# Performance work log

Hardware: AMD Instinct MI355X
Metric: run time of the kernel (lower is better)

The kernel has to match this reference:

```python
import jax, jax.numpy as jnp
import numpy as np

HID = 2048      # hidden_size
NH = 32         # num_heads
QLR = 1536      # q_lora_rank
KVLR = 512      # kv_lora_rank
DR = 64         # qk_rope_head_dim
DN = 128        # qk_nope_head_dim
DV = 128        # v_head_dim
DQK = DN + DR   # 192
EPS = 1e-6
ROPE_BASE = 10000.0


def rms_norm(x, w):
    return x * jax.lax.rsqrt(jnp.mean(x * x, axis=-1, keepdims=True) + EPS) * w


def apply_rope(x, pos):
    # x: [B, S, H, d] (non-interleaved / rotate-half convention), pos: [S]
    d = x.shape[-1]
    inv_freq = 1.0 / (ROPE_BASE ** (jnp.arange(0, d, 2, dtype=jnp.float32) / d))
    freqs = pos[:, None].astype(jnp.float32) * inv_freq      # [S, d/2]
    cos = jnp.cos(freqs)[None, :, None, :]                   # [1, S, 1, d/2]
    sin = jnp.sin(freqs)[None, :, None, :]
    x1, x2 = x[..., : d // 2], x[..., d // 2:]
    return jnp.concatenate([x1 * cos - x2 * sin, x1 * sin + x2 * cos], axis=-1)


def setup_inputs() -> dict:
    key = jax.random.key(0)
    ks = jax.random.split(key, 8)
    s = 0.02
    return {
        "hidden_states": jax.random.normal(ks[0], (1, 2048, HID), jnp.float32),
        "q_a_w":    jax.random.normal(ks[1], (HID, QLR), jnp.float32) * s,
        "q_a_ln_w": jnp.ones((QLR,), jnp.float32),
        "q_b_w":    jax.random.normal(ks[2], (QLR, NH * DQK), jnp.float32) * s,
        "kv_a_w":   jax.random.normal(ks[3], (HID, KVLR + DR), jnp.float32) * s,
        "kv_a_ln_w": jnp.ones((KVLR,), jnp.float32),
        "kv_b_w":   jax.random.normal(ks[4], (KVLR, NH * (DN + DV)), jnp.float32) * s,
        "o_w":      jax.random.normal(ks[5], (NH * DV, HID), jnp.float32) * s,
    }


def reference(hidden_states, q_a_w, q_a_ln_w, q_b_w, kv_a_w, kv_a_ln_w, kv_b_w, o_w):
    B, S, _ = hidden_states.shape
    # low-rank Q: down-proj -> RMSNorm -> up-proj
    q = rms_norm(hidden_states @ q_a_w, q_a_ln_w) @ q_b_w       # [B,S,NH*DQK]
    q = q.reshape(B, S, NH, DQK)
    q_pass, q_rot = q[..., :DN], q[..., DN:]
    # compressed KV + shared rope key
    ckv = hidden_states @ kv_a_w                                # [B,S,KVLR+DR]
    c_kv, k_rot = ckv[..., :KVLR], ckv[..., KVLR:]
    kv = rms_norm(c_kv, kv_a_ln_w) @ kv_b_w                     # [B,S,NH*(DN+DV)]
    kv = kv.reshape(B, S, NH, DN + DV)
    k_pass, v = kv[..., :DN], kv[..., DN:]
    # RoPE
    pos = jnp.arange(S)
    q_rot = apply_rope(q_rot, pos)                              # [B,S,NH,DR]
    k_rot = apply_rope(k_rot[:, :, None, :], pos)[:, :, 0, :]   # [B,S,DR] (shared head)
    # causal attention, scale = qk_head_dim**-0.5
    scale = DQK ** -0.5
    scores = (jnp.einsum('bqhd,bkhd->bhqk', q_pass, k_pass)
              + jnp.einsum('bqhd,bkd->bhqk', q_rot, k_rot)) * scale
    causal = jnp.tril(jnp.ones((S, S), dtype=bool))
    scores = jnp.where(causal[None, None], scores, jnp.finfo(scores.dtype).min)
    p = jax.nn.softmax(scores, axis=-1)
    out = jnp.einsum('bhqk,bkhd->bqhd', p, v).reshape(B, S, NH * DV)
    return out @ o_w
```

## Files before the change

kernel.cpp:

```cpp
#include <hip/hip_runtime.h>


typedef __bf16 bf16x8 __attribute__((ext_vector_type(8)));
typedef float  f32x4  __attribute__((ext_vector_type(4)));
typedef unsigned u32x4 __attribute__((ext_vector_type(4)));

#define GLOAD16(g, l)                                                          \
  __builtin_amdgcn_global_load_lds(                                            \
      (const __attribute__((address_space(1))) unsigned int*)(g),              \
      (__attribute__((address_space(3))) unsigned int*)(l), 16, 0, 0)

__device__ __forceinline__ unsigned short f2b(float f) {
  unsigned u = __builtin_bit_cast(unsigned, f);
  u += 0x7fffu + ((u >> 16) & 1u);
  return (unsigned short)(u >> 16);
}

__device__ __forceinline__ float b2f(unsigned short u) {
  return __builtin_bit_cast(float, (unsigned)u << 16);
}

__device__ __forceinline__ unsigned cvtpk(float lo, float hi) {
  unsigned r;
  asm("v_cvt_pk_bf16_f32 %0, %1, %2" : "=v"(r) : "v"(lo), "v"(hi));
  return r;
}

__device__ __forceinline__ void tc_body(const float* __restrict__ src,
                                        unsigned short* __restrict__ dst,
                                        int R, int C, int bx, int by,
                                        int tx, int ty) {
  __shared__ float t[32][33];
  int r0 = bx * 32, c0 = by * 32;
#pragma unroll
  for (int j = 0; j < 4; j++) {
    int c = c0 + tx;
    t[ty + j * 8][tx] = (c < C) ? src[(size_t)(r0 + ty + j * 8) * C + c] : 0.f;
  }
  __syncthreads();
#pragma unroll
  for (int j = 0; j < 4; j++)
    dst[(size_t)(c0 + ty + j * 8) * R + r0 + tx] = f2b(t[tx][ty + j * 8]);
}

__global__ __launch_bounds__(256) void prep(
    const float* __restrict__ hs, unsigned short* __restrict__ hs_b,
    const float* __restrict__ qaw, const float* __restrict__ kvaw,
    unsigned short* __restrict__ wcat,
    const float* __restrict__ qbw, unsigned short* __restrict__ qbT,
    const float* __restrict__ kvbw, unsigned short* __restrict__ kvbT,
    const float* __restrict__ ow, unsigned short* __restrict__ owT) {
  int b = blockIdx.x;
  int tid = threadIdx.x;
  if (b < 4096) {
    int i = b * 256 + tid;
    float4 v = ((const float4*)hs)[i];
    ushort4 o;
    o.x = f2b(v.x); o.y = f2b(v.y); o.z = f2b(v.z); o.w = f2b(v.w);
    ((ushort4*)hs_b)[i] = o;
    return;
  }
  b -= 4096;
  int tx = tid & 31, ty = tid >> 5;
  if (b < 3072)       { tc_body(qaw,  wcat,               2048, 1536, b & 63,  b >> 6, tx, ty); return; }
  b -= 3072;
  if (b < 1280)       { tc_body(kvaw, wcat + 1536UL*2048, 2048, 576,  b & 63,  b >> 6, tx, ty); return; }
  b -= 1280;
  if (b < 9216)       { tc_body(qbw,  qbT,                1536, 6144, b % 48,  b / 48, tx, ty); return; }
  b -= 9216;
  if (b < 4096)       { tc_body(kvbw, kvbT,               512,  8192, b & 15,  b >> 4, tx, ty); return; }
  b -= 4096;
  tc_body(ow, owT, 4096, 2048, b & 127, b >> 7, tx, ty);
}

__global__ __launch_bounds__(256) void rms2(const float* __restrict__ c0,
                                            const float* __restrict__ c1,
                                            const float* __restrict__ qw,
                                            const float* __restrict__ kvw,
                                            unsigned short* __restrict__ qan,
                                            unsigned short* __restrict__ ckvn,
                                            unsigned short* __restrict__ Kb) {
  int b = blockIdx.x, tid = threadIdx.x;
  __shared__ float red[4];
  if (b < 2048) {
    const float* x0 = c0 + (size_t)b * 2176;
    const float* x1 = c1 + (size_t)b * 2176;
    float vb[6], ss = 0.f;
#pragma unroll
    for (int j = 0; j < 6; j++) {
      float v = x0[tid + j * 256] + x1[tid + j * 256];
      vb[j] = v; ss += v * v;
    }
#pragma unroll
    for (int off = 1; off < 64; off <<= 1) ss += __shfl_xor(ss, off, 64);
    if ((tid & 63) == 0) red[tid >> 6] = ss;
    __syncthreads();
    ss = red[0] + red[1] + red[2] + red[3];
    float r = rsqrtf(ss / 1536.f + 1e-6f);
    unsigned short* orow = qan + (size_t)b * 1536;
#pragma unroll
    for (int j = 0; j < 6; j++)
      orow[tid + j * 256] = f2b(vb[j] * r * qw[tid + j * 256]);
  } else {
    int t = b - 2048;
    const float* x0 = c0 + (size_t)t * 2176 + 1536;
    const float* x1 = c1 + (size_t)t * 2176 + 1536;
    float vb[2], ss = 0.f;
#pragma unroll
    for (int j = 0; j < 2; j++) {
      float v = x0[tid + j * 256] + x1[tid + j * 256];
      vb[j] = v; ss += v * v;
    }
#pragma unroll
    for (int off = 1; off < 64; off <<= 1) ss += __shfl_xor(ss, off, 64);
    __shared__ unsigned short rot[64];
    if ((tid & 63) == 0) red[tid >> 6] = ss;
    __syncthreads();
    ss = red[0] + red[1] + red[2] + red[3];
    float r = rsqrtf(ss / 512.f + 1e-6f);
    unsigned short* orow = ckvn + (size_t)t * 512;
#pragma unroll
    for (int j = 0; j < 2; j++)
      orow[tid + j * 256] = f2b(vb[j] * r * kvw[tid + j * 256]);
    if (tid < 32) {
      float x1v = c0[(size_t)t * 2176 + 2048 + tid] + c1[(size_t)t * 2176 + 2048 + tid];
      float x2v = c0[(size_t)t * 2176 + 2080 + tid] + c1[(size_t)t * 2176 + 2080 + tid];
      float a = (float)t * exp2f(-(float)tid * 0.4152410118609203f);
      float cs = __cosf(a), sn = __sinf(a);
      rot[tid]      = f2b(x1v * cs - x2v * sn);
      rot[tid + 32] = f2b(x1v * sn + x2v * cs);
    }
    __syncthreads();
    for (int idx = tid; idx < 2048; idx += 256) {
      int h = idx >> 6, d = idx & 63;
      Kb[(size_t)t * 6144 + h * 192 + 128 + d] = rot[d];
    }
  }
}

__global__ __launch_bounds__(256) void addout(const float4* __restrict__ p,
                                              float4* __restrict__ o) {
  int i = blockIdx.x * 256 + threadIdx.x;
  float4 a = p[i], b = p[i + 1048576], c = p[i + 2097152], d = p[i + 3145728];
  float4 r;
  r.x = (a.x + b.x) + (c.x + d.x);
  r.y = (a.y + b.y) + (c.y + d.y);
  r.z = (a.z + b.z) + (c.z + d.z);
  r.w = (a.w + b.w) + (c.w + d.w);
  o[i] = r;
}

__global__ __launch_bounds__(256) void gemm_bt(const unsigned short* __restrict__ A,
                                               const unsigned short* __restrict__ Bt,
                                               float* __restrict__ Cp,
                                               int M, int N, int Ktot,
                                               int GX, int total, int splits) {
  __shared__ unsigned short As[4096];
  __shared__ unsigned short Bs[4096];
  const int tid = threadIdx.x;
  const int w = tid >> 6, lane = tid & 63;
  const int lr = lane & 15, lh = lane >> 4;
  const int lin = blockIdx.x, cpx = gridDim.x >> 3;
  int sid = (lin & 7) * cpx + (lin >> 3);
  const int s = sid / total;
  sid -= s * total;
  const int m0 = (sid / GX) * 128, n0 = (sid % GX) * 128;
  const int Kseg = Ktot / splits;
  const unsigned short* Ab = A + (size_t)s * Kseg;
  const unsigned short* Bb = Bt + (size_t)s * Kseg;
  float* C = Cp + (size_t)s * M * N;
  const int wm = w >> 1, wn = w & 1;
  const int srow = lane >> 2;
  const int schunk = (lane & 3) ^ ((lane >> 3) & 3);
  const int swzr = (lr >> 1) & 3;

  f32x4 acc[4][4];
  const f32x4 z = {0.f, 0.f, 0.f, 0.f};
#pragma unroll
  for (int i = 0; i < 4; i++)
#pragma unroll
    for (int j = 0; j < 4; j++) acc[i][j] = z;

  for (int k0 = 0; k0 < Kseg; k0 += 32) {
#pragma unroll
    for (int c = 0; c < 2; c++) {
      GLOAD16(Ab + (size_t)(m0 + c * 64 + w * 16 + srow) * Ktot + k0 + schunk * 8,
              As + c * 2048 + w * 512);
      GLOAD16(Bb + (size_t)(n0 + c * 64 + w * 16 + srow) * Ktot + k0 + schunk * 8,
              Bs + c * 2048 + w * 512);
    }
    __syncthreads();
    bf16x8 a[4], b[4];
#pragma unroll
    for (int m = 0; m < 4; m++) {
      int row = wm * 64 + m * 16 + lr;
      a[m] = *(const bf16x8*)(As + row * 32 + ((lh ^ swzr) * 8));
    }
#pragma unroll
    for (int n = 0; n < 4; n++) {
      int row = wn * 64 + n * 16 + lr;
      b[n] = *(const bf16x8*)(Bs + row * 32 + ((lh ^ swzr) * 8));
    }
#pragma unroll
    for (int m = 0; m < 4; m++)
#pragma unroll
      for (int n = 0; n < 4; n++)
        acc[m][n] = __builtin_amdgcn_mfma_f32_16x16x32_bf16(a[m], b[n], acc[m][n], 0, 0, 0);
    __syncthreads();
  }
#pragma unroll
  for (int m = 0; m < 4; m++)
#pragma unroll
    for (int n = 0; n < 4; n++)
#pragma unroll
      for (int r = 0; r < 4; r++) {
        int row = m0 + wm * 64 + m * 16 + lh * 4 + r;
        int col = n0 + wn * 64 + n * 16 + lr;
        C[(size_t)row * N + col] = acc[m][n][r];
      }
}

__global__ __launch_bounds__(512) void gemm256m(
    const unsigned short* __restrict__ Aq, const unsigned short* __restrict__ Bq,
    unsigned short* __restrict__ Qb,
    const unsigned short* __restrict__ Akv, const unsigned short* __restrict__ Bkv,
    unsigned short* __restrict__ Kb, unsigned short* __restrict__ Vt) {
  __shared__ unsigned short lds[2][2][16384];
  const int tid = threadIdx.x;
  const int w = tid >> 6, lane = tid & 63;
  const int lr = lane & 15, lh = lane >> 4;
  const int wr = w >> 2, wc = w & 3;
  const int blk = blockIdx.x;
  const bool isq = blk < 192;
  const int bx = isq ? (blk % 24) : ((blk - 192) & 31);
  const int by = isq ? (blk / 24) : ((blk - 192) >> 5);
  const int K  = isq ? 1536 : 512;
  const unsigned short* A  = isq ? Aq : Akv;
  const unsigned short* Bt = isq ? Bq : Bkv;
  const int m0 = by * 256, n0 = bx * 256;

  int soff[2];
#pragma unroll
  for (int j = 0; j < 2; j++) {
    int c = j * 512 + tid;
    int row = c >> 3, p = c & 7;
    soff[j] = row * K + (p ^ (row & 7)) * 8;
  }
  const unsigned short* Abase = A + (size_t)m0 * K;
  const unsigned short* Bbase = Bt + (size_t)n0 * K;
  const int rswz = lr & 7;

#define STAGEOP(op, Base, kt, buf)                                             \
  {                                                                            \
    _Pragma("unroll") for (int hh = 0; hh < 2; hh++)                           \
    _Pragma("unroll") for (int j = 0; j < 2; j++)                              \
      GLOAD16(Base + (size_t)(hh * 128) * K + soff[j] + (kt) * 64,             \
              &lds[buf][op][(hh * 1024 + j * 512 + w * 64) * 8]);              \
  }
#define READA(mh, buf)                                                         \
  {                                                                            \
    _Pragma("unroll") for (int mi = 0; mi < 4; mi++)                           \
    _Pragma("unroll") for (int ks = 0; ks < 2; ks++)                           \
      af[mi][ks] = *(const bf16x8*)&lds[buf][0][                               \
          (wr * 128 + ((mh) * 4 + mi) * 16 + lr) * 64 +                        \
          (((ks * 4 + lh) ^ rswz) * 8)];                                       \
  }
#define READB(n, buf)                                                          \
  {                                                                            \
    _Pragma("unroll") for (int ks = 0; ks < 2; ks++)                           \
      bfr[n][ks] = *(const bf16x8*)&lds[buf][1][                               \
          (wc * 64 + (n) * 16 + lr) * 64 + (((ks * 4 + lh) ^ rswz) * 8)];      \
  }
#define MFMAQ(mh, nh)                                                          \
  {                                                                            \
    __builtin_amdgcn_s_setprio(1);                                             \
    _Pragma("unroll") for (int mi = 0; mi < 4; mi++)                           \
    _Pragma("unroll") for (int ni = 0; ni < 2; ni++)                           \
    _Pragma("unroll") for (int ks = 0; ks < 2; ks++)                           \
      acc[(mh) * 4 + mi][(nh) * 2 + ni] =                                      \
          __builtin_amdgcn_mfma_f32_16x16x32_bf16(                             \
              af[mi][ks], bfr[(nh) * 2 + ni][ks],                              \
              acc[(mh) * 4 + mi][(nh) * 2 + ni], 0, 0, 0);                     \
    __builtin_amdgcn_s_setprio(0);                                             \
  }

  f32x4 acc[8][4];
  const f32x4 z = {0.f, 0.f, 0.f, 0.f};
#pragma unroll
  for (int i = 0; i < 8; i++)
#pragma unroll
    for (int j = 0; j < 4; j++) acc[i][j] = z;

  STAGEOP(0, Abase, 0, 0);
  STAGEOP(1, Bbase, 0, 0);
  asm volatile("s_waitcnt vmcnt(0)" ::: "memory");
  __builtin_amdgcn_s_barrier();

  const int KT = K >> 6;
  for (int kt = 0; kt < KT; ++kt) {
    const int buf = kt & 1;
    const bool more = (kt + 1 < KT);
    bf16x8 af[4][2], bfr[4][2];
    READA(0, buf);
    READB(0, buf); READB(1, buf);
    if (more) STAGEOP(0, Abase, kt + 1, buf ^ 1);
    __builtin_amdgcn_s_barrier();
    MFMAQ(0, 0);
    __builtin_amdgcn_s_barrier();
    READB(2, buf); READB(3, buf);
    if (more) STAGEOP(1, Bbase, kt + 1, buf ^ 1);
    __builtin_amdgcn_s_barrier();
    MFMAQ(0, 1);
    __builtin_amdgcn_s_barrier();
    READA(1, buf);
    __builtin_amdgcn_s_barrier();
    MFMAQ(1, 1);
    __builtin_amdgcn_s_barrier();
    MFMAQ(1, 0);
    if (more) asm volatile("s_waitcnt vmcnt(0)" ::: "memory");
    __builtin_amdgcn_s_barrier();
  }
#undef STAGEOP
#undef READA
#undef READB
#undef MFMAQ

  if (isq) {
    const float kSc = 0.104126984f;
#pragma unroll
    for (int m = 0; m < 8; m++)
#pragma unroll
      for (int n = 0; n < 4; n++) {
        int colb = n0 + wc * 64 + n * 16;
        int sb = colb % 192;
        bool isrope = sb >= 128;
        bool first  = sb < 160;
        int col = colb + lr;
#pragma unroll
        for (int r = 0; r < 4; r++) {
          int row = m0 + wr * 128 + m * 16 + lh * 4 + r;
          float v = acc[m][n][r], o;
          if (!isrope) {
            o = v;
          } else {
            int ii = (col - 128) & 31;
            float ang = (float)row * exp2f(-(float)ii * 0.4152410118609203f);
            float cs = __cosf(ang), sn = __sinf(ang);
            float pa_ = acc[m][(n + 2) & 3][r];
            float pb_ = acc[m][(n + 6) & 3][r];
            float partner = first ? pa_ : pb_;
            o = first ? (v * cs - partner * sn) : (partner * sn + v * cs);
          }
          Qb[(size_t)row * 6144 + col] = f2b(o * kSc);
        }
      }
  } else {
    const int h = bx;
    unsigned short* Vlds = (unsigned short*)lds;
    if (wc < 2) {
#pragma unroll
      for (int m = 0; m < 8; m++)
#pragma unroll
        for (int n = 0; n < 4; n++) {
          int dd = wc * 64 + n * 16 + lr;
          int rowb = m0 + wr * 128 + m * 16 + lh * 4;
#pragma unroll
          for (int r = 0; r < 4; r++)
            Kb[(size_t)(rowb + r) * 6144 + h * 192 + dd] = f2b(acc[m][n][r]);
        }
    } else {
#pragma unroll
      for (int m = 0; m < 8; m++)
#pragma unroll
        for (int n = 0; n < 4; n++) {
          int dd = (wc - 2) * 64 + n * 16 + lr;
          int tl = wr * 128 + m * 16 + lh * 4;
          ushort4 pk;
          pk.x = f2b(acc[m][n][0]); pk.y = f2b(acc[m][n][1]);
          pk.z = f2b(acc[m][n][2]); pk.w = f2b(acc[m][n][3]);
          *(ushort4*)(Vlds + dd * 264 + tl) = pk;
        }
    }
    __syncthreads();
    {
      int r = tid >> 2, seg = tid & 3;
      const unsigned short* srcp = Vlds + r * 264 + seg * 64;
      unsigned short* dstp = Vt + (size_t)(h * 128 + r) * 2048 + m0 + seg * 64;
#pragma unroll
      for (int j = 0; j < 8; j++)
        *(int4*)(dstp + j * 8) = *(const int4*)(srcp + j * 8);
    }
  }
}

__global__ __launch_bounds__(512) void gemm256_op(
    const unsigned short* __restrict__ A, const unsigned short* __restrict__ Bt,
    float* __restrict__ Cp) {
  __shared__ unsigned short lds[2][2][16384];
  const int tid = threadIdx.x;
  const int w = tid >> 6, lane = tid & 63;
  const int lr = lane & 15, lh = lane >> 4;
  const int wr = w >> 2, wc = w & 3;
  const int lin = blockIdx.x;
  const int sid = (lin & 7) * 32 + (lin >> 3);
  const int s = sid >> 6, rem = sid & 63;
  const int m0 = (rem >> 3) * 256, n0 = (rem & 7) * 256;
  const int Kst = 4096;
  const int koff = s * 1024;

  int soff[2];
#pragma unroll
  for (int j = 0; j < 2; j++) {
    int c = j * 512 + tid;
    int row = c >> 3, p = c & 7;
    soff[j] = row * Kst + (p ^ (row & 7)) * 8;
  }
  const unsigned short* Abase = A + (size_t)m0 * Kst + koff;
  const unsigned short* Bbase = Bt + (size_t)n0 * Kst + koff;
  const int rswz = lr & 7;

#define STAGEOP(op, Base, kt, buf)                                             \
  {                                                                            \
    _Pragma("unroll") for (int hh = 0; hh < 2; hh++)                           \
    _Pragma("unroll") for (int j = 0; j < 2; j++)                              \
      GLOAD16(Base + (size_t)(hh * 128) * Kst + soff[j] + (kt) * 64,           \
              &lds[buf][op][(hh * 1024 + j * 512 + w * 64) * 8]);              \
  }
#define READA(mh, buf)                                                         \
  {                                                                            \
    _Pragma("unroll") for (int mi = 0; mi < 4; mi++)                           \
    _Pragma("unroll") for (int ks = 0; ks < 2; ks++)                           \
      af[mi][ks] = *(const bf16x8*)&lds[buf][0][                               \
          (wr * 128 + ((mh) * 4 + mi) * 16 + lr) * 64 +                        \
          (((ks * 4 + lh) ^ rswz) * 8)];                                       \
  }
#define READB(n, buf)                                                         \
  {                                                                            \
    _Pragma("unroll") for (int ks = 0; ks < 2; ks++)                           \
      bfr[n][ks] = *(const bf16x8*)&lds[buf][1][                               \
          (wc * 64 + (n) * 16 + lr) * 64 + (((ks * 4 + lh) ^ rswz) * 8)];      \
  }
#define MFMAQ(mh, nh)                                                          \
  {                                                                            \
    __builtin_amdgcn_s_setprio(1);                                             \
    _Pragma("unroll") for (int mi = 0; mi < 4; mi++)                           \
    _Pragma("unroll") for (int ni = 0; ni < 2; ni++)                           \
    _Pragma("unroll") for (int ks = 0; ks < 2; ks++)                           \
      acc[(mh) * 4 + mi][(nh) * 2 + ni] =                                      \
          __builtin_amdgcn_mfma_f32_16x16x32_bf16(                             \
              af[mi][ks], bfr[(nh) * 2 + ni][ks],                              \
              acc[(mh) * 4 + mi][(nh) * 2 + ni], 0, 0, 0);                     \
    __builtin_amdgcn_s_setprio(0);                                             \
  }

  f32x4 acc[8][4];
  const f32x4 z = {0.f, 0.f, 0.f, 0.f};
#pragma unroll
  for (int i = 0; i < 8; i++)
#pragma unroll
    for (int j = 0; j < 4; j++) acc[i][j] = z;

  STAGEOP(0, Abase, 0, 0);
  STAGEOP(1, Bbase, 0, 0);
  asm volatile("s_waitcnt vmcnt(0)" ::: "memory");
  __builtin_amdgcn_s_barrier();

  const int KT = 16;
  for (int kt = 0; kt < KT; ++kt) {
    const int buf = kt & 1;
    const bool more = (kt + 1 < KT);
    bf16x8 af[4][2], bfr[4][2];
    READA(0, buf);
    READB(0, buf); READB(1, buf);
    if (more) STAGEOP(0, Abase, kt + 1, buf ^ 1);
    __builtin_amdgcn_s_barrier();
    MFMAQ(0, 0);
    __builtin_amdgcn_s_barrier();
    READB(2, buf); READB(3, buf);
    if (more) STAGEOP(1, Bbase, kt + 1, buf ^ 1);
    __builtin_amdgcn_s_barrier();
    MFMAQ(0, 1);
    __builtin_amdgcn_s_barrier();
    READA(1, buf);
    __builtin_amdgcn_s_barrier();
    MFMAQ(1, 1);
    __builtin_amdgcn_s_barrier();
    MFMAQ(1, 0);
    if (more) asm volatile("s_waitcnt vmcnt(0)" ::: "memory");
    __builtin_amdgcn_s_barrier();
  }
#undef STAGEOP
#undef READA
#undef READB
#undef MFMAQ

  float* C = Cp + (size_t)s * 2048 * 2048;
#pragma unroll
  for (int m = 0; m < 8; m++)
#pragma unroll
    for (int n = 0; n < 4; n++)
#pragma unroll
      for (int r = 0; r < 4; r++) {
        int row = m0 + wr * 128 + m * 16 + lh * 4 + r;
        int col = n0 + wc * 64 + n * 16 + lr;
        C[(size_t)row * 2048 + col] = acc[m][n][r];
      }
}

__global__ __launch_bounds__(512) void attn(const unsigned short* __restrict__ Qb,
                                            const unsigned short* __restrict__ Kb,
                                            const unsigned short* __restrict__ Vt,
                                            unsigned short* __restrict__ Po,
                                            float* __restrict__ Ml) {
  __shared__ unsigned short Kl[2][6144];
  __shared__ unsigned short Vl[2][4096];
  const int tid = threadIdx.x;
  const int w = tid >> 6, lane = tid & 63;
  const int lr = lane & 15, lh = lane >> 4;
  const int b = blockIdx.x;
  const int x = b & 7, r_ = b >> 3;
  const int h = x + 8 * (r_ & 3);
  const int p = r_ >> 2;
  const int a = p >> 1, par = p & 1;

  const unsigned short* Kbase = Kb + h * 192;
  const unsigned short* Vbase = Vt + (size_t)h * 128 * 2048;
  size_t kga0, kga1 = 0;
  {
    int c = w * 64 + lane;
    int rr = c / 24, pp = c - rr * 24;
    kga0 = (size_t)rr * 6144 + (pp ^ (rr & 7)) * 8;
  }
  if (w < 4) {
    int c = 512 + w * 64 + lane;
    int rr = c / 24, pp = c - rr * 24;
    kga1 = (size_t)rr * 6144 + (pp ^ (rr & 7)) * 8;
  }
  size_t vga;
  {
    int c = w * 64 + lane;
    int d = c >> 2, pp = c & 3;
    vga = (size_t)d * 2048 + (pp ^ ((d >> 1) & 3)) * 8;
  }

#define STAGE(T0, B)                                                           \
  {                                                                            \
    GLOAD16(Kbase + (size_t)(T0) * 6144 + kga0, &Kl[B][w * 512]);              \
    if (w < 4)                                                                 \
      GLOAD16(Kbase + (size_t)(T0) * 6144 + kga1, &Kl[B][4096 + w * 512]);     \
    GLOAD16(Vbase + vga + (T0), &Vl[B][w * 512]);                              \
  }

  const int swz = (lr & 7) * 8;
  const int vsw = (lh ^ ((lr >> 1) & 3)) * 8;
  const int sA = lr + 32 * (lh & 1), sB = sA + 16;
  const f32x4 z = {0.f, 0.f, 0.f, 0.f};

  for (int job = 0; job < 2; ++job) {
    const int qi = job ? (15 - a) : a;
    const int q0 = qi << 7;
    const int qw = q0 + w * 16;
    const int qv = qw + lr;
    const int cnt = 2 * (qi + 1);

    bf16x8 qf[6];
#pragma unroll
    for (int cc = 0; cc < 6; cc++)
      qf[cc] = *(const bf16x8*)(Qb + (size_t)(qw + lr) * 6144 + h * 192 + cc * 32 + lh * 8);

    f32x4 acc[8];
#pragma unroll
    for (int n = 0; n < 8; n++) acc[n] = z;
    float lrow = 0.f;

    STAGE((size_t)(par) << 5, 0);
    __syncthreads();
    for (int k = 0; k < cnt; ++k) {
      const int t0 = (par + 2 * k) << 5;
      const int cur = k & 1;
      if (k + 1 < cnt) STAGE((size_t)(par + 2 * (k + 1)) << 5, cur ^ 1);
      if (t0 <= qw + 15) {
        f32x4 s0 = z, s1 = z;
        __builtin_amdgcn_s_setprio(1);
#pragma unroll
        for (int cc = 0; cc < 6; cc++) {
          int col = ((cc * 4 + lh) * 8) ^ swz;
          bf16x8 k0 = *(const bf16x8*)(&Kl[cur][lr * 192 + col]);
          bf16x8 k1 = *(const bf16x8*)(&Kl[cur][(16 + lr) * 192 + col]);
          s0 = __builtin_amdgcn_mfma_f32_16x16x32_bf16(k0, qf[cc], s0, 0, 0, 0);
          s1 = __builtin_amdgcn_mfma_f32_16x16x32_bf16(k1, qf[cc], s1, 0, 0, 0);
        }
        __builtin_amdgcn_s_setprio(0);
        const int tb = t0 + lh * 4;
        if (t0 + 31 > qw) {
#pragma unroll
          for (int r = 0; r < 4; r++) {
            s0[r] = (tb + r > qv)      ? -1e30f : s0[r];
            s1[r] = (tb + 16 + r > qv) ? -1e30f : s1[r];
          }
        }
        float p0[4], p1[4], ls = 0.f;
#pragma unroll
        for (int r = 0; r < 4; r++) {
          p0[r] = exp2f(s0[r]);
          p1[r] = exp2f(s1[r]);
          ls += p0[r] + p1[r];
        }
        lrow += ls;
        unsigned pk0 = cvtpk(p0[0], p0[1]), pk1 = cvtpk(p0[2], p0[3]);
        unsigned pk2 = cvtpk(p1[0], p1[1]), pk3 = cvtpk(p1[2], p1[3]);
        unsigned A0 = __shfl(pk0, sA, 64), A1 = __shfl(pk1, sA, 64);
        unsigned B0 = __shfl(pk0, sB, 64), B1 = __shfl(pk1, sB, 64);
        unsigned C0 = __shfl(pk2, sA, 64), C1 = __shfl(pk3, sA, 64);
        unsigned D0 = __shfl(pk2, sB, 64), D1 = __shfl(pk3, sB, 64);
        u32x4 pw;
        pw[0] = (lh < 2) ? A0 : C0;
        pw[1] = (lh < 2) ? A1 : C1;
        pw[2] = (lh < 2) ? B0 : D0;
        pw[3] = (lh < 2) ? B1 : D1;
        bf16x8 pa = __builtin_bit_cast(bf16x8, pw);
        __builtin_amdgcn_s_setprio(1);
#pragma unroll
        for (int n = 0; n < 8; n++) {
          bf16x8 vb = *(const bf16x8*)(&Vl[cur][(n * 16 + lr) * 32 + vsw]);
          acc[n] = __builtin_amdgcn_mfma_f32_16x16x32_bf16(pa, vb, acc[n], 0, 0, 0);
        }
        __builtin_amdgcn_s_setprio(0);
      }
      __syncthreads();
    }
    lrow += __shfl_xor(lrow, 16, 64);
    lrow += __shfl_xor(lrow, 32, 64);
    float invL = (lrow > 0.f) ? (1.f / lrow) : 0.f;
    float inv[4];
#pragma unroll
    for (int r = 0; r < 4; r++) inv[r] = __shfl(invL, lh * 4 + r, 16);
    unsigned short* Pob = Po + (size_t)par * 8388608;
#pragma unroll
    for (int n = 0; n < 8; n++)
#pragma unroll
      for (int r = 0; r < 4; r++) {
        int q = qw + lh * 4 + r;
        Pob[(size_t)q * 4096 + h * 128 + n * 16 + lr] = f2b(acc[n][r] * inv[r]);
      }
    if (lh == 0)
      Ml[(size_t)par * 65536 + h * 2048 + qw + lr] = lrow;
  }
#undef STAGE
}

__global__ __launch_bounds__(256) void combine(const unsigned short* __restrict__ Po,
                                               const float* __restrict__ Ml,
                                               unsigned short* __restrict__ Out) {
  int gid = blockIdx.x * 256 + threadIdx.x;
  int row = gid >> 4, seg = gid & 15;
  int q = row >> 5, h = row & 31;
  float l0 = Ml[h * 2048 + q];
  float l1 = Ml[65536 + h * 2048 + q];
  float inv = 1.f / (l0 + l1);
  float w0 = l0 * inv, w1 = l1 * inv;
  size_t off = (size_t)q * 4096 + h * 128 + seg * 8;
  ushort4 a0 = *(const ushort4*)(Po + off);
  ushort4 a1 = *(const ushort4*)(Po + off + 4);
  ushort4 b0 = *(const ushort4*)(Po + 8388608 + off);
  ushort4 b1 = *(const ushort4*)(Po + 8388608 + off + 4);
  ushort4 o0, o1;
  o0.x = f2b(w0 * b2f(a0.x) + w1 * b2f(b0.x));
  o0.y = f2b(w0 * b2f(a0.y) + w1 * b2f(b0.y));
  o0.z = f2b(w0 * b2f(a0.z) + w1 * b2f(b0.z));
  o0.w = f2b(w0 * b2f(a0.w) + w1 * b2f(b0.w));
  o1.x = f2b(w0 * b2f(a1.x) + w1 * b2f(b1.x));
  o1.y = f2b(w0 * b2f(a1.y) + w1 * b2f(b1.y));
  o1.z = f2b(w0 * b2f(a1.z) + w1 * b2f(b1.z));
  o1.w = f2b(w0 * b2f(a1.w) + w1 * b2f(b1.w));
  *(ushort4*)(Out + off) = o0;
  *(ushort4*)(Out + off + 4) = o1;
}

extern "C" void kernel_launch(void* const* d_in, const int* in_sizes, int n_in,
                              void* d_out, int out_size, void* d_ws, size_t ws_size,
                              hipStream_t stream) {
  const float* hs      = (const float*)d_in[0];
  const float* q_a_w   = (const float*)d_in[1];
  const float* q_a_ln  = (const float*)d_in[2];
  const float* q_b_w   = (const float*)d_in[3];
  const float* kv_a_w  = (const float*)d_in[4];
  const float* kv_a_ln = (const float*)d_in[5];
  const float* kv_b_w  = (const float*)d_in[6];
  const float* o_w     = (const float*)d_in[7];
  float* out = (float*)d_out;

  char* ws = (char*)d_ws;
  size_t off = 0;
  auto alloc = [&](size_t bytes) {
    void* p = ws + off;
    off += (bytes + 255) & ~(size_t)255;
    return p;
  };
  unsigned short* wcat    = (unsigned short*)alloc(2176UL * 2048 * 2);
  unsigned short* q_b_wT  = (unsigned short*)alloc(6144UL * 1536 * 2);
  unsigned short* kv_b_wT = (unsigned short*)alloc(8192UL * 512 * 2);
  unsigned short* o_wT    = (unsigned short*)alloc(2048UL * 4096 * 2);
  unsigned short* hs_b    = (unsigned short*)alloc(2048UL * 2048 * 2);
  unsigned short* q_a_n   = (unsigned short*)alloc(2048UL * 1536 * 2);
  unsigned short* Qb      = (unsigned short*)alloc(2048UL * 6144 * 2);
  unsigned short* ckv_n   = (unsigned short*)alloc(2048UL * 512 * 2);
  unsigned short* Kb      = (unsigned short*)alloc(2048UL * 6144 * 2);
  unsigned short* Vt      = (unsigned short*)alloc(32UL * 128 * 2048 * 2);
  float*          OutP    = (float*)Qb;
  char* big = (char*)alloc(2UL * 2048 * 2176 * 4);
  float*          Craw0    = (float*)big;
  float*          Craw1    = (float*)(big + 2048UL * 2176 * 4);
  unsigned short* Po       = (unsigned short*)big;
  float*          Ml       = (float*)alloc(2UL * 32 * 2048 * 4);
  unsigned short* attn_out = (unsigned short*)alloc(2048UL * 4096 * 2);
  (void)ws_size; (void)in_sizes; (void)n_in; (void)out_size;

  dim3 b256(256), b512(512);
  prep<<<29952, b256, 0, stream>>>(hs, hs_b, q_a_w, kv_a_w, wcat,
                                   q_b_w, q_b_wT, kv_b_w, kv_b_wT, o_w, o_wT);
  gemm_bt<<<544, b256, 0, stream>>>(hs_b, wcat, Craw0, 2048, 2176, 2048, 17, 272, 2);
  rms2<<<4096, b256, 0, stream>>>(Craw0, Craw1, q_a_ln, kv_a_ln, q_a_n, ckv_n, Kb);
  gemm256m<<<448, b512, 0, stream>>>(q_a_n, q_b_wT, Qb, ckv_n, kv_b_wT, Kb, Vt);
  attn<<<512, b512, 0, stream>>>(Qb, Kb, Vt, Po, Ml);
  combine<<<4096, b256, 0, stream>>>(Po, Ml, attn_out);
  gemm256_op<<<256, b512, 0, stream>>>(attn_out, o_wT, OutP);
  addout<<<4096, b256, 0, stream>>>((const float4*)OutP, (float4*)out);
}
```

Baseline: 278.7 us.

## Switch 256x256 GEMMs to 4-stage K=32 pipeline with single barrier per step

```diff
diff --git a/kernel.cpp b/kernel.cpp
--- a/kernel.cpp
+++ b/kernel.cpp
@@ -220,12 +220,46 @@
       }
 }
 
+#define G256_CORE32(KT)                                                        \
+  const int rcol = (lh ^ ((lr >> 1) & 3)) * 8;                                 \
+  f32x4 acc[8][4];                                                             \
+  {                                                                            \
+    const f32x4 zz = {0.f, 0.f, 0.f, 0.f};                                     \
+    _Pragma("unroll") for (int i = 0; i < 8; i++)                              \
+    _Pragma("unroll") for (int j = 0; j < 4; j++) acc[i][j] = zz;              \
+  }                                                                            \
+  STAGE32(0, 0);                                                               \
+  STAGE32(1, 1);                                                               \
+  STAGE32(2, 2);                                                               \
+  asm volatile("s_waitcnt vmcnt(8)" ::: "memory");                             \
+  __builtin_amdgcn_s_barrier();                                                \
+  for (int kt = 0; kt < (KT); ++kt) {                                          \
+    const int buf = kt & 3;                                                    \
+    if (kt + 3 < (KT)) STAGE32(kt + 3, (kt + 3) & 3);                          \
+    bf16x8 af[8], bfr[4];                                                      \
+    _Pragma("unroll") for (int f = 0; f < 8; f++)                              \
+      af[f] = *(const bf16x8*)&lds[buf][0][(wr * 128 + f * 16 + lr) * 32 + rcol]; \
+    _Pragma("unroll") for (int n = 0; n < 4; n++)                              \
+      bfr[n] = *(const bf16x8*)&lds[buf][1][(wc * 64 + n * 16 + lr) * 32 + rcol]; \
+    __builtin_amdgcn_s_setprio(1);                                             \
+    _Pragma("unroll") for (int f = 0; f < 8; f++)                              \
+    _Pragma("unroll") for (int n = 0; n < 4; n++)                              \
+      acc[f][n] = __builtin_amdgcn_mfma_f32_16x16x32_bf16(af[f], bfr[n],       \
+                                                          acc[f][n], 0, 0, 0); \
+    __builtin_amdgcn_s_setprio(0);                                             \
+    const int rem = (KT) - 1 - kt;                                             \
+    if (rem >= 3)      asm volatile("s_waitcnt vmcnt(8)" ::: "memory");        \
+    else if (rem == 2) asm volatile("s_waitcnt vmcnt(4)" ::: "memory");        \
+    else if (rem == 1) asm volatile("s_waitcnt vmcnt(0)" ::: "memory");        \
+    __builtin_amdgcn_s_barrier();                                              \
+  }
+
 __global__ __launch_bounds__(512) void gemm256m(
     const unsigned short* __restrict__ Aq, const unsigned short* __restrict__ Bq,
     unsigned short* __restrict__ Qb,
     const unsigned short* __restrict__ Akv, const unsigned short* __restrict__ Bkv,
     unsigned short* __restrict__ Kb, unsigned short* __restrict__ Vt) {
-  __shared__ unsigned short lds[2][2][16384];
+  __shared__ unsigned short lds[4][2][8192];
   const int tid = threadIdx.x;
   const int w = tid >> 6, lane = tid & 63;
   const int lr = lane & 15, lh = lane >> 4;
@@ -238,92 +272,28 @@
   const unsigned short* A  = isq ? Aq : Akv;
   const unsigned short* Bt = isq ? Bq : Bkv;
   const int m0 = by * 256, n0 = bx * 256;
+  const unsigned short* Abase = A + (size_t)m0 * K;
+  const unsigned short* Bbase = Bt + (size_t)n0 * K;
 
   int soff[2];
 #pragma unroll
   for (int j = 0; j < 2; j++) {
     int c = j * 512 + tid;
-    int row = c >> 3, p = c & 7;
-    soff[j] = row * K + (p ^ (row & 7)) * 8;
-  }
-  const unsigned short* Abase = A + (size_t)m0 * K;
-  const unsigned short* Bbase = Bt + (size_t)n0 * K;
-  const int rswz = lr & 7;
-
-#define STAGEOP(op, Base, kt, buf)                                             \
+    int row = c >> 2, p = c & 3;
+    soff[j] = row * K + (p ^ ((row >> 1) & 3)) * 8;
+  }
+
+#define STAGE32(kt, buf)                                                       \
   {                                                                            \
-    _Pragma("unroll") for (int hh = 0; hh < 2; hh++)                           \
-    _Pragma("unroll") for (int j = 0; j < 2; j++)                              \
-      GLOAD16(Base + (size_t)(hh * 128) * K + soff[j] + (kt) * 64,             \
-              &lds[buf][op][(hh * 1024 + j * 512 + w * 64) * 8]);              \
-  }
-#define READA(mh, buf)                                                         \
-  {                                                                            \
-    _Pragma("unroll") for (int mi = 0; mi < 4; mi++)                           \
-    _Pragma("unroll") for (int ks = 0; ks < 2; ks++)                           \
-      af[mi][ks] = *(const bf16x8*)&lds[buf][0][                               \
-          (wr * 128 + ((mh) * 4 + mi) * 16 + lr) * 64 +                        \
-          (((ks * 4 + lh) ^ rswz) * 8)];                                       \
-  }
-#define READB(n, buf)                                                          \
-  {                                                                            \
-    _Pragma("unroll") for (int ks = 0; ks < 2; ks++)                           \
-      bfr[n][ks] = *(const bf16x8*)&lds[buf][1][                               \
-          (wc * 64 + (n) * 16 + lr) * 64 + (((ks * 4 + lh) ^ rswz) * 8)];      \
-  }
-#define MFMAQ(mh, nh)                                                          \
-  {                                                                            \
-    __builtin_amdgcn_s_setprio(1);                                             \
-    _Pragma("unroll") for (int mi = 0; mi < 4; mi++)                           \
-    _Pragma("unroll") for (int ni = 0; ni < 2; ni++)                           \
-    _Pragma("unroll") for (int ks = 0; ks < 2; ks++)                           \
-      acc[(mh) * 4 + mi][(nh) * 2 + ni] =                                      \
-          __builtin_amdgcn_mfma_f32_16x16x32_bf16(                             \
-              af[mi][ks], bfr[(nh) * 2 + ni][ks],                              \
-              acc[(mh) * 4 + mi][(nh) * 2 + ni], 0, 0, 0);                     \
-    __builtin_amdgcn_s_setprio(0);                                             \
-  }
-
-  f32x4 acc[8][4];
-  const f32x4 z = {0.f, 0.f, 0.f, 0.f};
-#pragma unroll
-  for (int i = 0; i < 8; i++)
-#pragma unroll
-    for (int j = 0; j < 4; j++) acc[i][j] = z;
-
-  STAGEOP(0, Abase, 0, 0);
-  STAGEOP(1, Bbase, 0, 0);
-  asm volatile("s_waitcnt vmcnt(0)" ::: "memory");
-  __builtin_amdgcn_s_barrier();
-
-  const int KT = K >> 6;
-  for (int kt = 0; kt < KT; ++kt) {
-    const int buf = kt & 1;
-    const bool more = (kt + 1 < KT);
-    bf16x8 af[4][2], bfr[4][2];
-    READA(0, buf);
-    READB(0, buf); READB(1, buf);
-    if (more) STAGEOP(0, Abase, kt + 1, buf ^ 1);
-    __builtin_amdgcn_s_barrier();
-    MFMAQ(0, 0);
-    __builtin_amdgcn_s_barrier();
-    READB(2, buf); READB(3, buf);
-    if (more) STAGEOP(1, Bbase, kt + 1, buf ^ 1);
-    __builtin_amdgcn_s_barrier();
-    MFMAQ(0, 1);
-    __builtin_amdgcn_s_barrier();
-    READA(1, buf);
-    __builtin_amdgcn_s_barrier();
-    MFMAQ(1, 1);
-    __builtin_amdgcn_s_barrier();
-    MFMAQ(1, 0);
-    if (more) asm volatile("s_waitcnt vmcnt(0)" ::: "memory");
-    __builtin_amdgcn_s_barrier();
-  }
-#undef STAGEOP
-#undef READA
-#undef READB
-#undef MFMAQ
+    _Pragma("unroll") for (int j = 0; j < 2; j++) {                            \
+      GLOAD16(Abase + soff[j] + (kt) * 32, &lds[buf][0][(j * 512 + tid) * 8]); \
+      GLOAD16(Bbase + soff[j] + (kt) * 32, &lds[buf][1][(j * 512 + tid) * 8]); \
+    }                                                                          \
+  }
+
+  const int KT = K >> 5;
+  G256_CORE32(KT)
+#undef STAGE32
 
   if (isq) {
     const float kSc = 0.104126984f;
@@ -396,103 +366,38 @@
 __global__ __launch_bounds__(512) void gemm256_op(
     const unsigned short* __restrict__ A, const unsigned short* __restrict__ Bt,
     float* __restrict__ Cp) {
-  __shared__ unsigned short lds[2][2][16384];
+  __shared__ unsigned short lds[4][2][8192];
   const int tid = threadIdx.x;
   const int w = tid >> 6, lane = tid & 63;
   const int lr = lane & 15, lh = lane >> 4;
   const int wr = w >> 2, wc = w & 3;
   const int lin = blockIdx.x;
   const int sid = (lin & 7) * 32 + (lin >> 3);
-  const int s = sid >> 6, rem = sid & 63;
-  const int m0 = (rem >> 3) * 256, n0 = (rem & 7) * 256;
+  const int s = sid >> 6, rem_ = sid & 63;
+  const int m0 = (rem_ >> 3) * 256, n0 = (rem_ & 7) * 256;
   const int Kst = 4096;
   const int koff = s * 1024;
+  const unsigned short* Abase = A + (size_t)m0 * Kst + koff;
+  const unsigned short* Bbase = Bt + (size_t)n0 * Kst + koff;
 
   int soff[2];
 #pragma unroll
   for (int j = 0; j < 2; j++) {
     int c = j * 512 + tid;
-    int row = c >> 3, p = c & 7;
-    soff[j] = row * Kst + (p ^ (row & 7)) * 8;
-  }
-  const unsigned short* Abase = A + (size_t)m0 * Kst + koff;
-  const unsigned short* Bbase = Bt + (size_t)n0 * Kst + koff;
-  const int rswz = lr & 7;
-
-#define STAGEOP(op, Base, kt, buf)                                             \
+    int row = c >> 2, p = c & 3;
+    soff[j] = row * Kst + (p ^ ((row >> 1) & 3)) * 8;
+  }
+
+#define STAGE32(kt, buf)                                                       \
   {                                                                            \
-    _Pragma("unroll") for (int hh = 0; hh < 2; hh++)                           \
-    _Pragma("unroll") for (int j = 0; j < 2; j++)                              \
-      GLOAD16(Base + (size_t)(hh * 128) * Kst + soff[j] + (kt) * 64,           \
-              &lds[buf][op][(hh * 1024 + j * 512 + w * 64) * 8]);              \
-  }
-#define READA(mh, buf)                                                         \
-  {                                                                            \
-    _Pragma("unroll") for (int mi = 0; mi < 4; mi++)                           \
-    _Pragma("unroll") for (int ks = 0; ks < 2; ks++)                           \
-      af[mi][ks] = *(const bf16x8*)&lds[buf][0][                               \
-          (wr * 128 + ((mh) * 4 + mi) * 16 + lr) * 64 +                        \
-          (((ks * 4 + lh) ^ rswz) * 8)];                                       \
-  }
-#define READB(n, buf)                                                         \
-  {                                                                            \
-    _Pragma("unroll") for (int ks = 0; ks < 2; ks++)                           \
-      bfr[n][ks] = *(const bf16x8*)&lds[buf][1][                               \
-          (wc * 64 + (n) * 16 + lr) * 64 + (((ks * 4 + lh) ^ rswz) * 8)];      \
-  }
-#define MFMAQ(mh, nh)                                                          \
-  {                                                                            \
-    __builtin_amdgcn_s_setprio(1);                                             \
-    _Pragma("unroll") for (int mi = 0; mi < 4; mi++)                           \
-    _Pragma("unroll") for (int ni = 0; ni < 2; ni++)                           \
-    _Pragma("unroll") for (int ks = 0; ks < 2; ks++)                           \
-      acc[(mh) * 4 + mi][(nh) * 2 + ni] =                                      \
-          __builtin_amdgcn_mfma_f32_16x16x32_bf16(                             \
-              af[mi][ks], bfr[(nh) * 2 + ni][ks],                              \
-              acc[(mh) * 4 + mi][(nh) * 2 + ni], 0, 0, 0);                     \
-    __builtin_amdgcn_s_setprio(0);                                             \
-  }
-
-  f32x4 acc[8][4];
-  const f32x4 z = {0.f, 0.f, 0.f, 0.f};
-#pragma unroll
-  for (int i = 0; i < 8; i++)
-#pragma unroll
-    for (int j = 0; j < 4; j++) acc[i][j] = z;
-
-  STAGEOP(0, Abase, 0, 0);
-  STAGEOP(1, Bbase, 0, 0);
-  asm volatile("s_waitcnt vmcnt(0)" ::: "memory");
-  __builtin_amdgcn_s_barrier();
-
-  const int KT = 16;
-  for (int kt = 0; kt < KT; ++kt) {
-    const int buf = kt & 1;
-    const bool more = (kt + 1 < KT);
-    bf16x8 af[4][2], bfr[4][2];
-    READA(0, buf);
-    READB(0, buf); READB(1, buf);
-    if (more) STAGEOP(0, Abase, kt + 1, buf ^ 1);
-    __builtin_amdgcn_s_barrier();
-    MFMAQ(0, 0);
-    __builtin_amdgcn_s_barrier();
-    READB(2, buf); READB(3, buf);
-    if (more) STAGEOP(1, Bbase, kt + 1, buf ^ 1);
-    __builtin_amdgcn_s_barrier();
-    MFMAQ(0, 1);
-    __builtin_amdgcn_s_barrier();
-    READA(1, buf);
-    __builtin_amdgcn_s_barrier();
-    MFMAQ(1, 1);
-    __builtin_amdgcn_s_barrier();
-    MFMAQ(1, 0);
-    if (more) asm volatile("s_waitcnt vmcnt(0)" ::: "memory");
-    __builtin_amdgcn_s_barrier();
-  }
-#undef STAGEOP
-#undef READA
-#undef READB
-#undef MFMAQ
+    _Pragma("unroll") for (int j = 0; j < 2; j++) {                            \
+      GLOAD16(Abase + soff[j] + (kt) * 32, &lds[buf][0][(j * 512 + tid) * 8]); \
+      GLOAD16(Bbase + soff[j] + (kt) * 32, &lds[buf][1][(j * 512 + tid) * 8]); \
+    }                                                                          \
+  }
+
+  G256_CORE32(32)
+#undef STAGE32
 
   float* C = Cp + (size_t)s * 2048 * 2048;
 #pragma unroll
```

After: 284.6 us. 1.02x slower.
